# Kernel tuning notes

Measured on AMD Instinct MI355X. Metric: run time of the kernel, lower is better.

## Reference

```python
import jax, jax.numpy as jnp
import numpy as np

NUM_GRAPHS = 4
INPUT_SIZE = 50000          # nodes per graph
BOTTLENECK = 64
FFN = 128
HIDDEN = [1, 8, 16]         # hidden_channels; convs go 16->8 then 8->1
E = 3200000                 # num edges (avg degree 16)
N = NUM_GRAPHS * INPUT_SIZE # total nodes = 200000


def setup_inputs() -> dict:
    key = jax.random.key(0)
    ks = jax.random.split(key, 12)
    d = {}
    d["x"] = jax.random.normal(ks[0], (NUM_GRAPHS, BOTTLENECK), dtype=jnp.float32)
    d["edge_index"] = jax.random.randint(ks[1], (2, E), 0, N, dtype=jnp.int64)
    d["edge_weight"] = jax.random.uniform(ks[2], (E,), dtype=jnp.float32)
    # learned params (stored as [in, out] so forward is x @ W + b)
    d["fc1_w"] = jax.random.normal(ks[3], (BOTTLENECK, FFN), dtype=jnp.float32) / np.sqrt(BOTTLENECK)
    d["fc1_b"] = jnp.zeros((FFN,), dtype=jnp.float32)
    d["fc2_w"] = jax.random.normal(ks[4], (FFN, INPUT_SIZE * HIDDEN[-1]), dtype=jnp.float32) / np.sqrt(FFN)
    d["fc2_b"] = jnp.zeros((INPUT_SIZE * HIDDEN[-1],), dtype=jnp.float32)
    d["conv0_w"] = jax.random.normal(ks[5], (HIDDEN[2], HIDDEN[1]), dtype=jnp.float32) / np.sqrt(HIDDEN[2])
    d["conv0_b"] = jnp.zeros((HIDDEN[1],), dtype=jnp.float32)
    d["conv1_w"] = jax.random.normal(ks[6], (HIDDEN[1], HIDDEN[0]), dtype=jnp.float32) / np.sqrt(HIDDEN[1])
    d["conv1_b"] = jnp.zeros((HIDDEN[0],), dtype=jnp.float32)
    d["num_graphs"] = NUM_GRAPHS
    return d


def _gcn_conv(x, row, col, ew, W, b, n_nodes):
    """PyG GCNConv: add self loops (weight 1), symmetric normalization,
    scatter-add of normalized source features, then linear weight + bias."""
    loop = jnp.arange(n_nodes, dtype=row.dtype)
    r = jnp.concatenate([row, loop])
    c = jnp.concatenate([col, loop])
    w = jnp.concatenate([ew, jnp.ones((n_nodes,), dtype=ew.dtype)])
    deg = jax.ops.segment_sum(w, c, num_segments=n_nodes)          # [N]
    dinv = jnp.where(deg > 0, jax.lax.rsqrt(deg), 0.0)
    norm = dinv[r] * w * dinv[c]                                    # [E+N]
    h = x @ W                                                       # [N, out]
    msg = h[r] * norm[:, None]                                      # gather + scale
    out = jax.ops.segment_sum(msg, c, num_segments=n_nodes)        # scatter-add
    return out + b


def reference(x, edge_index, edge_weight, fc1_w, fc1_b, fc2_w, fc2_b,
              conv0_w, conv0_b, conv1_w, conv1_b, num_graphs):
    act = jax.nn.elu
    row, col = edge_index[0], edge_index[1]
    n_nodes = num_graphs * INPUT_SIZE
    z = act(x @ fc1_w + fc1_b)                                     # [G, ffn]
    z = act(z @ fc2_w + fc2_b)                                     # [G, input_size*hidden[-1]]
    h = z.reshape(n_nodes, HIDDEN[-1])                             # [N, 16]
    out = _gcn_conv(h, row, col, edge_weight, conv0_w, conv0_b, n_nodes)  # 16->8
    out = act(out)                                                 # act except last layer
    out = _gcn_conv(out, row, col, edge_weight, conv1_w, conv1_b, n_nodes)  # 8->1
    return out
```

## Files before the change

kernel.cpp:

```cpp
#include <hip/hip_runtime.h>
#include <cstddef>

#define NGRAPH  4
#define NPG     50000
#define NNODES  200000
#define BNECK   64
#define FFN     128
#define COLS    800000
#define NEDGE   3200000
#define H2      16
#define H1      8

#define MAXDEG  40
#define OVCAP   8192
#define RANGES  16
#define RW      (NNODES / RANGES)
#define EPB     4096
#define CH      ((NEDGE + EPB - 1) / EPB)

#define SCAN_B  512
#define NB      ((NNODES + SCAN_B - 1) / SCAN_B)

__device__ __forceinline__ float elu(float x) {
    return x > 0.f ? x : expm1f(x);
}

__global__ void k_fc1(const float* __restrict__ x, const float* __restrict__ w,
                      const float* __restrict__ b, float* __restrict__ z1) {
    int t = threadIdx.x;
    int g = t >> 7, j = t & 127;
    float acc = b[j];
    #pragma unroll 8
    for (int i = 0; i < BNECK; ++i)
        acc = fmaf(x[g * BNECK + i], w[i * FFN + j], acc);
    z1[t] = elu(acc);
}

__global__ void k_zero(int* __restrict__ p, int n) {
    int i = blockIdx.x * blockDim.x + threadIdx.x;
    if (i < n) p[i] = 0;
}

__global__ void k_place_ell(const int* __restrict__ row, const int* __restrict__ col,
                            const float* __restrict__ ew,
                            int* __restrict__ cnt, int2* __restrict__ ell,
                            int* __restrict__ ovc, int3* __restrict__ ovf) {
    int b = blockIdx.x;
    int x = b & 7;
    int q = b >> 3;
    int p = q / CH;
    int chunk = q - p * CH;
    int c0 = (p * 8 + x) * RW;
    int c1 = c0 + RW;
    int base = chunk * EPB;
    #pragma unroll
    for (int i = 0; i < EPB / 256; ++i) {
        int e = base + i * 256 + threadIdx.x;
        if (e < NEDGE) {
            int c = col[e];
            if (c >= c0 && c < c1) {
                int pos = atomicAdd(&cnt[c], 1);
                if (pos < MAXDEG) {
                    int2 ent; ent.x = row[e]; ent.y = __float_as_int(ew[e]);
                    ell[(size_t)c * MAXDEG + pos] = ent;
                } else {
                    int o = atomicAdd(ovc, 1);
                    if (o < OVCAP) {
                        int3 ent3; ent3.x = c; ent3.y = row[e]; ent3.z = __float_as_int(ew[e]);
                        ovf[o] = ent3;
                    }
                }
            }
        }
    }
}

__global__ void k_deg_ell(const int* __restrict__ cnt, const int2* __restrict__ ell,
                          const int* __restrict__ ovc, const int3* __restrict__ ovf,
                          float* __restrict__ dinv) {
    int n = blockIdx.x * blockDim.x + threadIdx.x;
    if (n >= NNODES) return;
    int d = cnt[n];
    int m = d < MAXDEG ? d : MAXDEG;
    const int2* en = &ell[(size_t)n * MAXDEG];
    float s = 1.0f;
    for (int j = 0; j < m; ++j) s += __int_as_float(en[j].y);
    if (d > MAXDEG) {
        int oc = *ovc; if (oc > OVCAP) oc = OVCAP;
        for (int j = 0; j < oc; ++j)
            if (ovf[j].x == n) s += __int_as_float(ovf[j].z);
    }
    dinv[n] = rsqrtf(s);
}

__global__ __launch_bounds__(256) void k_fc2(
    const float* __restrict__ z1, const float* __restrict__ w2,
    const float* __restrict__ b2, const float* __restrict__ cw0,
    const float* __restrict__ dinv,
    float* __restrict__ hws, float* __restrict__ acc0)
{
    __shared__ float s_z1[NGRAPH * FFN];
    __shared__ float s_cw[H2 * H1];
    __shared__ float s_h[NGRAPH][1024];

    int t = threadIdx.x;
    for (int i = t; i < NGRAPH * FFN; i += 256) s_z1[i] = z1[i];
    if (t < H2 * H1) s_cw[t] = cw0[t];
    __syncthreads();

    int j0 = blockIdx.x * 1024;
    int jj = j0 + t * 4;
    if (jj < COLS) {
        float4 a0 = {0,0,0,0}, a1 = {0,0,0,0}, a2 = {0,0,0,0}, a3 = {0,0,0,0};
        #pragma unroll 4
        for (int i = 0; i < FFN; ++i) {
            const float4 wv = *reinterpret_cast<const float4*>(&w2[(size_t)i * COLS + jj]);
            float zg0 = s_z1[0 * FFN + i];
            float zg1 = s_z1[1 * FFN + i];
            float zg2 = s_z1[2 * FFN + i];
            float zg3 = s_z1[3 * FFN + i];
            a0.x = fmaf(zg0, wv.x, a0.x); a0.y = fmaf(zg0, wv.y, a0.y);
            a0.z = fmaf(zg0, wv.z, a0.z); a0.w = fmaf(zg0, wv.w, a0.w);
            a1.x = fmaf(zg1, wv.x, a1.x); a1.y = fmaf(zg1, wv.y, a1.y);
            a1.z = fmaf(zg1, wv.z, a1.z); a1.w = fmaf(zg1, wv.w, a1.w);
            a2.x = fmaf(zg2, wv.x, a2.x); a2.y = fmaf(zg2, wv.y, a2.y);
            a2.z = fmaf(zg2, wv.z, a2.z); a2.w = fmaf(zg2, wv.w, a2.w);
            a3.x = fmaf(zg3, wv.x, a3.x); a3.y = fmaf(zg3, wv.y, a3.y);
            a3.z = fmaf(zg3, wv.z, a3.z); a3.w = fmaf(zg3, wv.w, a3.w);
        }
        const float4 bv = *reinterpret_cast<const float4*>(&b2[jj]);
        s_h[0][t*4+0] = elu(a0.x + bv.x); s_h[0][t*4+1] = elu(a0.y + bv.y);
        s_h[0][t*4+2] = elu(a0.z + bv.z); s_h[0][t*4+3] = elu(a0.w + bv.w);
        s_h[1][t*4+0] = elu(a1.x + bv.x); s_h[1][t*4+1] = elu(a1.y + bv.y);
        s_h[1][t*4+2] = elu(a1.z + bv.z); s_h[1][t*4+3] = elu(a1.w + bv.w);
        s_h[2][t*4+0] = elu(a2.x + bv.x); s_h[2][t*4+1] = elu(a2.y + bv.y);
        s_h[2][t*4+2] = elu(a2.z + bv.z); s_h[2][t*4+3] = elu(a2.w + bv.w);
        s_h[3][t*4+0] = elu(a3.x + bv.x); s_h[3][t*4+1] = elu(a3.y + bv.y);
        s_h[3][t*4+2] = elu(a3.z + bv.z); s_h[3][t*4+3] = elu(a3.w + bv.w);
    }
    __syncthreads();

    int nbase = j0 >> 4;
    for (int o = t; o < NGRAPH * 64 * H1; o += 256) {
        int g  = o >> 9;
        int lo = o & 511;
        int nl = lo >> 3;
        int m  = lo & 7;
        int nloc = nbase + nl;
        if (nloc < NPG) {
            const float* hr = &s_h[g][nl * 16];
            float s = 0.f;
            #pragma unroll
            for (int k = 0; k < H2; ++k) s = fmaf(hr[k], s_cw[k * H1 + m], s);
            int node = g * NPG + nloc;
            float di = dinv[node];
            hws[node * H1 + m]  = s * di;
            acc0[node * H1 + m] = s * (di * di);
        }
    }
}

__global__ void k_gather0_ell(const int* __restrict__ cnt, const int2* __restrict__ ell,
                              const int* __restrict__ ovc, const int3* __restrict__ ovf,
                              const float* __restrict__ hws, const float* __restrict__ acc0,
                              const float* __restrict__ b0, const float* __restrict__ cw1,
                              const float* __restrict__ dinv, float* __restrict__ h1s) {
    int n = blockIdx.x * blockDim.x + threadIdx.x;
    if (n >= NNODES) return;
    int d = cnt[n];
    int m = d < MAXDEG ? d : MAXDEG;
    const int2* en = &ell[(size_t)n * MAXDEG];
    float4 mA = {0,0,0,0}, mB = {0,0,0,0};
    for (int j = 0; j < m; ++j) {
        int2 ent = en[j];
        float w = __int_as_float(ent.y);
        const float4 ha = *reinterpret_cast<const float4*>(&hws[ent.x * H1]);
        const float4 hb = *reinterpret_cast<const float4*>(&hws[ent.x * H1 + 4]);
        mA.x = fmaf(ha.x, w, mA.x); mA.y = fmaf(ha.y, w, mA.y);
        mA.z = fmaf(ha.z, w, mA.z); mA.w = fmaf(ha.w, w, mA.w);
        mB.x = fmaf(hb.x, w, mB.x); mB.y = fmaf(hb.y, w, mB.y);
        mB.z = fmaf(hb.z, w, mB.z); mB.w = fmaf(hb.w, w, mB.w);
    }
    if (d > MAXDEG) {
        int oc = *ovc; if (oc > OVCAP) oc = OVCAP;
        for (int j = 0; j < oc; ++j) {
            if (ovf[j].x == n) {
                float w = __int_as_float(ovf[j].z);
                int r = ovf[j].y;
                const float4 ha = *reinterpret_cast<const float4*>(&hws[r * H1]);
                const float4 hb = *reinterpret_cast<const float4*>(&hws[r * H1 + 4]);
                mA.x = fmaf(ha.x, w, mA.x); mA.y = fmaf(ha.y, w, mA.y);
                mA.z = fmaf(ha.z, w, mA.z); mA.w = fmaf(ha.w, w, mA.w);
                mB.x = fmaf(hb.x, w, mB.x); mB.y = fmaf(hb.y, w, mB.y);
                mB.z = fmaf(hb.z, w, mB.z); mB.w = fmaf(hb.w, w, mB.w);
            }
        }
    }
    float dc = dinv[n];
    const float4 sA = *reinterpret_cast<const float4*>(&acc0[n * H1]);
    const float4 sB = *reinterpret_cast<const float4*>(&acc0[n * H1 + 4]);
    float s = 0.f;
    s = fmaf(elu(sA.x + dc * mA.x + b0[0]), cw1[0], s);
    s = fmaf(elu(sA.y + dc * mA.y + b0[1]), cw1[1], s);
    s = fmaf(elu(sA.z + dc * mA.z + b0[2]), cw1[2], s);
    s = fmaf(elu(sA.w + dc * mA.w + b0[3]), cw1[3], s);
    s = fmaf(elu(sB.x + dc * mB.x + b0[4]), cw1[4], s);
    s = fmaf(elu(sB.y + dc * mB.y + b0[5]), cw1[5], s);
    s = fmaf(elu(sB.z + dc * mB.z + b0[6]), cw1[6], s);
    s = fmaf(elu(sB.w + dc * mB.w + b0[7]), cw1[7], s);
    h1s[n] = s * dc;
}

__global__ void k_gather1_ell(const int* __restrict__ cnt, const int2* __restrict__ ell,
                              const int* __restrict__ ovc, const int3* __restrict__ ovf,
                              const float* __restrict__ h1s, const float* __restrict__ dinv,
                              const float* __restrict__ cb1, float* __restrict__ out) {
    int n = blockIdx.x * blockDim.x + threadIdx.x;
    if (n >= NNODES) return;
    int d = cnt[n];
    int m = d < MAXDEG ? d : MAXDEG;
    const int2* en = &ell[(size_t)n * MAXDEG];
    float a = h1s[n];
    for (int j = 0; j < m; ++j) {
        int2 ent = en[j];
        a = fmaf(h1s[ent.x], __int_as_float(ent.y), a);
    }
    if (d > MAXDEG) {
        int oc = *ovc; if (oc > OVCAP) oc = OVCAP;
        for (int j = 0; j < oc; ++j)
            if (ovf[j].x == n) a = fmaf(h1s[ovf[j].y], __int_as_float(ovf[j].z), a);
    }
    out[n] = cb1[0] + a * dinv[n];
}

__global__ void k_hist(const int* __restrict__ col, int* __restrict__ cnt) {
    int e = blockIdx.x * blockDim.x + threadIdx.x;
    if (e < NEDGE) atomicAdd(&cnt[col[e]], 1);
}

__global__ void k_bsum(const int* __restrict__ cnt, int* __restrict__ bsum) {
    __shared__ int s[SCAN_B];
    int t = threadIdx.x;
    int i = blockIdx.x * SCAN_B + t;
    s[t] = (i < NNODES) ? cnt[i] : 0;
    __syncthreads();
    for (int st = SCAN_B / 2; st > 0; st >>= 1) {
        if (t < st) s[t] += s[t + st];
        __syncthreads();
    }
    if (t == 0) bsum[blockIdx.x] = s[0];
}

__global__ void k_btop(const int* __restrict__ bsum, int* __restrict__ bstart) {
    __shared__ int s[SCAN_B];
    int t = threadIdx.x;
    int v = (t < NB) ? bsum[t] : 0;
    s[t] = v;
    __syncthreads();
    for (int st = 1; st < SCAN_B; st <<= 1) {
        int x = (t >= st) ? s[t - st] : 0;
        __syncthreads();
        s[t] += x;
        __syncthreads();
    }
    if (t < NB) bstart[t] = s[t] - v;
}

__global__ void k_bscan(int* __restrict__ cnt, const int* __restrict__ bstart) {
    __shared__ int s[SCAN_B];
    int t = threadIdx.x;
    int i = blockIdx.x * SCAN_B + t;
    int v = (i < NNODES) ? cnt[i] : 0;
    s[t] = v;
    __syncthreads();
    for (int st = 1; st < SCAN_B; st <<= 1) {
        int x = (t >= st) ? s[t - st] : 0;
        __syncthreads();
        s[t] += x;
        __syncthreads();
    }
    if (i < NNODES) cnt[i] = bstart[blockIdx.x] + s[t] - v;
}

__global__ void k_place(const int* __restrict__ row, const int* __restrict__ col,
                        const float* __restrict__ ew,
                        int* __restrict__ offs, int2* __restrict__ csr) {
    int e = blockIdx.x * blockDim.x + threadIdx.x;
    if (e >= NEDGE) return;
    int c = col[e];
    int pos = atomicAdd(&offs[c], 1);
    int2 ent;
    ent.x = row[e];
    ent.y = __float_as_int(ew[e]);
    csr[pos] = ent;
}

__global__ void k_deg(const int* __restrict__ offs, const int2* __restrict__ csr,
                      float* __restrict__ dinv) {
    int n = blockIdx.x * blockDim.x + threadIdx.x;
    if (n >= NNODES) return;
    int s0 = n ? offs[n - 1] : 0;
    int e0 = offs[n];
    float d = 1.0f;
    for (int j = s0; j < e0; ++j) d += __int_as_float(csr[j].y);
    dinv[n] = rsqrtf(d);
}

__global__ void k_gather0(const int* __restrict__ offs, const int2* __restrict__ csr,
                          const float* __restrict__ hws, const float* __restrict__ acc0,
                          const float* __restrict__ b0, const float* __restrict__ cw1,
                          const float* __restrict__ dinv, float* __restrict__ h1s) {
    int n = blockIdx.x * blockDim.x + threadIdx.x;
    if (n >= NNODES) return;
    int s0 = n ? offs[n - 1] : 0;
    int e0 = offs[n];
    float4 mA = {0,0,0,0}, mB = {0,0,0,0};
    for (int j = s0; j < e0; ++j) {
        int2 ent = csr[j];
        int   r = ent.x;
        float w = __int_as_float(ent.y);
        const float4 ha = *reinterpret_cast<const float4*>(&hws[r * H1]);
        const float4 hb = *reinterpret_cast<const float4*>(&hws[r * H1 + 4]);
        mA.x = fmaf(ha.x, w, mA.x); mA.y = fmaf(ha.y, w, mA.y);
        mA.z = fmaf(ha.z, w, mA.z); mA.w = fmaf(ha.w, w, mA.w);
        mB.x = fmaf(hb.x, w, mB.x); mB.y = fmaf(hb.y, w, mB.y);
        mB.z = fmaf(hb.z, w, mB.z); mB.w = fmaf(hb.w, w, mB.w);
    }
    float dc = dinv[n];
    const float4 sA = *reinterpret_cast<const float4*>(&acc0[n * H1]);
    const float4 sB = *reinterpret_cast<const float4*>(&acc0[n * H1 + 4]);
    float s = 0.f;
    s = fmaf(elu(sA.x + dc * mA.x + b0[0]), cw1[0], s);
    s = fmaf(elu(sA.y + dc * mA.y + b0[1]), cw1[1], s);
    s = fmaf(elu(sA.z + dc * mA.z + b0[2]), cw1[2], s);
    s = fmaf(elu(sA.w + dc * mA.w + b0[3]), cw1[3], s);
    s = fmaf(elu(sB.x + dc * mB.x + b0[4]), cw1[4], s);
    s = fmaf(elu(sB.y + dc * mB.y + b0[5]), cw1[5], s);
    s = fmaf(elu(sB.z + dc * mB.z + b0[6]), cw1[6], s);
    s = fmaf(elu(sB.w + dc * mB.w + b0[7]), cw1[7], s);
    h1s[n] = s * dc;
}

__global__ void k_gather1(const int* __restrict__ offs, const int2* __restrict__ csr,
                          const float* __restrict__ h1s, const float* __restrict__ dinv,
                          const float* __restrict__ cb1, float* __restrict__ out) {
    int n = blockIdx.x * blockDim.x + threadIdx.x;
    if (n >= NNODES) return;
    int s0 = n ? offs[n - 1] : 0;
    int e0 = offs[n];
    float a = h1s[n];
    for (int j = s0; j < e0; ++j) {
        int2 ent = csr[j];
        a = fmaf(h1s[ent.x], __int_as_float(ent.y), a);
    }
    out[n] = cb1[0] + a * dinv[n];
}

extern "C" void kernel_launch(void* const* d_in, const int* in_sizes, int n_in,
                              void* d_out, int out_size, void* d_ws, size_t ws_size,
                              hipStream_t stream) {
    const float* x    = (const float*)d_in[0];
    const int*   ei   = (const int*)d_in[1];
    const float* ew   = (const float*)d_in[2];
    const float* fc1w = (const float*)d_in[3];
    const float* fc1b = (const float*)d_in[4];
    const float* fc2w = (const float*)d_in[5];
    const float* fc2b = (const float*)d_in[6];
    const float* cw0  = (const float*)d_in[7];
    const float* cb0  = (const float*)d_in[8];
    const float* cw1  = (const float*)d_in[9];
    const float* cb1  = (const float*)d_in[10];
    float* out = (float*)d_out;

    const int* row = ei;
    const int* col = ei + NEDGE;

    float* ws    = (float*)d_ws;
    float* z1    = ws;
    float* dinv  = ws + 512;
    float* hws   = dinv + NNODES;
    float* acc0  = hws + (size_t)NNODES * H1;
    float* h1s   = acc0 + (size_t)NNODES * H1;

    size_t ell_units = 512 + NNODES + 2u * (size_t)NNODES * H1 + NNODES
                     + (NNODES + 8) + (3u * OVCAP) + 2u * (size_t)NNODES * MAXDEG;
    bool use_ell = ws_size >= ell_units * 4u + 256u;

    if (use_ell) {
        int*  cnt = (int*)(h1s + NNODES);
        int*  ovc = cnt + NNODES;
        int3* ovf = (int3*)(ovc + 8);
        int2* ell = (int2*)((int*)ovf + 3 * OVCAP);

        k_fc1 <<<1, 512, 0, stream>>>(x, fc1w, fc1b, z1);
        k_zero<<<(NNODES + 8 + 255) / 256, 256, 0, stream>>>(cnt, NNODES + 8);
        k_place_ell<<<2 * CH * 8, 256, 0, stream>>>(row, col, ew, cnt, ell, ovc, ovf);
        k_deg_ell<<<(NNODES + 255) / 256, 256, 0, stream>>>(cnt, ell, ovc, ovf, dinv);
        k_fc2<<<(COLS + 1023) / 1024, 256, 0, stream>>>(z1, fc2w, fc2b, cw0, dinv, hws, acc0);
        k_gather0_ell<<<(NNODES + 255) / 256, 256, 0, stream>>>(cnt, ell, ovc, ovf, hws, acc0,
                                                                cb0, cw1, dinv, h1s);
        k_gather1_ell<<<(NNODES + 255) / 256, 256, 0, stream>>>(cnt, ell, ovc, ovf, h1s, dinv,
                                                                cb1, out);
    } else {
        int*   offs  = (int*)(h1s + NNODES);
        int*   bsum  = offs + NNODES;
        int*   bst   = bsum + SCAN_B;
        int2*  csr   = (int2*)(bst + SCAN_B);

        k_fc1 <<<1, 512, 0, stream>>>(x, fc1w, fc1b, z1);
        k_zero<<<(NNODES + 255) / 256, 256, 0, stream>>>(offs, NNODES);
        k_hist<<<(NEDGE + 255) / 256, 256, 0, stream>>>(col, offs);
        k_bsum<<<NB, SCAN_B, 0, stream>>>(offs, bsum);
        k_btop<<<1, SCAN_B, 0, stream>>>(bsum, bst);
        k_bscan<<<NB, SCAN_B, 0, stream>>>(offs, bst);
        k_place<<<(NEDGE + 255) / 256, 256, 0, stream>>>(row, col, ew, offs, csr);
        k_deg<<<(NNODES + 255) / 256, 256, 0, stream>>>(offs, csr, dinv);
        k_fc2<<<(COLS + 1023) / 1024, 256, 0, stream>>>(z1, fc2w, fc2b, cw0, dinv, hws, acc0);
        k_gather0<<<(NNODES + 255) / 256, 256, 0, stream>>>(offs, csr, hws, acc0, cb0, cw1, dinv, h1s);
        k_gather1<<<(NNODES + 255) / 256, 256, 0, stream>>>(offs, csr, h1s, dinv, cb1, out);
    }
}
```

Before: 952.1 us.

## Fuse init kernels, accumulate degree atomically, vectorize ELL edge reads

Merges fc1 and the zeroing into one init kernel. Degrees are now accumulated with float atomics during ELL placement, so the separate pass that re-read the ELL table is replaced by a trivial rsqrt kernel. The column reads in placement become int4 loads with larger chunks, and the gather kernels read ELL entries two at a time as int4. MAXDEG shrinks to 32, which saves memory but sends more edges to the overflow list, whose linear scan is costly for high-degree nodes. Float atomic ordering also makes degree sums nondeterministic.

```diff
diff --git a/kernel.cpp b/kernel.cpp
--- a/kernel.cpp
+++ b/kernel.cpp
@@ -11,11 +11,11 @@
 #define H2      16
 #define H1      8
 
-#define MAXDEG  40
+#define MAXDEG  32
 #define OVCAP   8192
 #define RANGES  16
 #define RW      (NNODES / RANGES)
-#define EPB     4096
+#define EPB     8192
 #define CH      ((NEDGE + EPB - 1) / EPB)
 
 #define SCAN_B  512
@@ -25,25 +25,29 @@
     return x > 0.f ? x : expm1f(x);
 }
 
-__global__ void k_fc1(const float* __restrict__ x, const float* __restrict__ w,
-                      const float* __restrict__ b, float* __restrict__ z1) {
-    int t = threadIdx.x;
-    int g = t >> 7, j = t & 127;
-    float acc = b[j];
-    #pragma unroll 8
-    for (int i = 0; i < BNECK; ++i)
-        acc = fmaf(x[g * BNECK + i], w[i * FFN + j], acc);
-    z1[t] = elu(acc);
-}
-
-__global__ void k_zero(int* __restrict__ p, int n) {
-    int i = blockIdx.x * blockDim.x + threadIdx.x;
-    if (i < n) p[i] = 0;
+__global__ void k_init(const float* __restrict__ x, const float* __restrict__ w,
+                       const float* __restrict__ b, float* __restrict__ z1,
+                       int* __restrict__ cnt, float* __restrict__ degf,
+                       int* __restrict__ ovc) {
+    if (blockIdx.x == 0) {
+        int t = threadIdx.x;
+        int g = t >> 7, j = t & 127;
+        float acc = b[j];
+        #pragma unroll 8
+        for (int i = 0; i < BNECK; ++i)
+            acc = fmaf(x[g * BNECK + i], w[i * FFN + j], acc);
+        z1[t] = elu(acc);
+        if (t == 0) *ovc = 0;
+    } else {
+        int i = (blockIdx.x - 1) * 512 + threadIdx.x;
+        if (i < NNODES) { cnt[i] = 0; degf[i] = 1.0f; }
+    }
 }
 
 __global__ void k_place_ell(const int* __restrict__ row, const int* __restrict__ col,
                             const float* __restrict__ ew,
-                            int* __restrict__ cnt, int2* __restrict__ ell,
+                            int* __restrict__ cnt, float* __restrict__ degf,
+                            int2* __restrict__ ell,
                             int* __restrict__ ovc, int3* __restrict__ ovf) {
     int b = blockIdx.x;
     int x = b & 7;
@@ -53,21 +57,29 @@
     int c0 = (p * 8 + x) * RW;
     int c1 = c0 + RW;
     int base = chunk * EPB;
+    const int4* col4 = reinterpret_cast<const int4*>(col);
     #pragma unroll
-    for (int i = 0; i < EPB / 256; ++i) {
-        int e = base + i * 256 + threadIdx.x;
+    for (int i = 0; i < EPB / 1024; ++i) {
+        int e = base + i * 1024 + threadIdx.x * 4;
         if (e < NEDGE) {
-            int c = col[e];
-            if (c >= c0 && c < c1) {
-                int pos = atomicAdd(&cnt[c], 1);
-                if (pos < MAXDEG) {
-                    int2 ent; ent.x = row[e]; ent.y = __float_as_int(ew[e]);
-                    ell[(size_t)c * MAXDEG + pos] = ent;
-                } else {
-                    int o = atomicAdd(ovc, 1);
-                    if (o < OVCAP) {
-                        int3 ent3; ent3.x = c; ent3.y = row[e]; ent3.z = __float_as_int(ew[e]);
-                        ovf[o] = ent3;
+            int4 c4 = col4[e >> 2];
+            #pragma unroll
+            for (int k = 0; k < 4; ++k) {
+                int c = (k == 0) ? c4.x : (k == 1) ? c4.y : (k == 2) ? c4.z : c4.w;
+                if (c >= c0 && c < c1) {
+                    int ee = e + k;
+                    float w = ew[ee];
+                    atomicAdd(&degf[c], w);
+                    int pos = atomicAdd(&cnt[c], 1);
+                    if (pos < MAXDEG) {
+                        int2 ent; ent.x = row[ee]; ent.y = __float_as_int(w);
+                        ell[(size_t)c * MAXDEG + pos] = ent;
+                    } else {
+                        int o = atomicAdd(ovc, 1);
+                        if (o < OVCAP) {
+                            int3 ent3; ent3.x = c; ent3.y = row[ee]; ent3.z = __float_as_int(w);
+                            ovf[o] = ent3;
+                        }
                     }
                 }
             }
@@ -75,22 +87,9 @@
     }
 }
 
-__global__ void k_deg_ell(const int* __restrict__ cnt, const int2* __restrict__ ell,
-                          const int* __restrict__ ovc, const int3* __restrict__ ovf,
-                          float* __restrict__ dinv) {
-    int n = blockIdx.x * blockDim.x + threadIdx.x;
-    if (n >= NNODES) return;
-    int d = cnt[n];
-    int m = d < MAXDEG ? d : MAXDEG;
-    const int2* en = &ell[(size_t)n * MAXDEG];
-    float s = 1.0f;
-    for (int j = 0; j < m; ++j) s += __int_as_float(en[j].y);
-    if (d > MAXDEG) {
-        int oc = *ovc; if (oc > OVCAP) oc = OVCAP;
-        for (int j = 0; j < oc; ++j)
-            if (ovf[j].x == n) s += __int_as_float(ovf[j].z);
-    }
-    dinv[n] = rsqrtf(s);
+__global__ void k_dinv(const float* __restrict__ degf, float* __restrict__ dinv) {
+    int n = blockIdx.x * blockDim.x + threadIdx.x;
+    if (n < NNODES) dinv[n] = rsqrtf(degf[n]);
 }
 
 __global__ __launch_bounds__(256) void k_fc2(
@@ -160,6 +159,16 @@
     }
 }
 
+__device__ __forceinline__ void acc_msg(int r, float w, const float* __restrict__ hws,
+                                        float4& mA, float4& mB) {
+    const float4 ha = *reinterpret_cast<const float4*>(&hws[r * H1]);
+    const float4 hb = *reinterpret_cast<const float4*>(&hws[r * H1 + 4]);
+    mA.x = fmaf(ha.x, w, mA.x); mA.y = fmaf(ha.y, w, mA.y);
+    mA.z = fmaf(ha.z, w, mA.z); mA.w = fmaf(ha.w, w, mA.w);
+    mB.x = fmaf(hb.x, w, mB.x); mB.y = fmaf(hb.y, w, mB.y);
+    mB.z = fmaf(hb.z, w, mB.z); mB.w = fmaf(hb.w, w, mB.w);
+}
+
 __global__ void k_gather0_ell(const int* __restrict__ cnt, const int2* __restrict__ ell,
                               const int* __restrict__ ovc, const int3* __restrict__ ovf,
                               const float* __restrict__ hws, const float* __restrict__ acc0,
@@ -169,32 +178,22 @@
     if (n >= NNODES) return;
     int d = cnt[n];
     int m = d < MAXDEG ? d : MAXDEG;
-    const int2* en = &ell[(size_t)n * MAXDEG];
+    const int4* en4 = reinterpret_cast<const int4*>(&ell[(size_t)n * MAXDEG]);
     float4 mA = {0,0,0,0}, mB = {0,0,0,0};
-    for (int j = 0; j < m; ++j) {
-        int2 ent = en[j];
-        float w = __int_as_float(ent.y);
-        const float4 ha = *reinterpret_cast<const float4*>(&hws[ent.x * H1]);
-        const float4 hb = *reinterpret_cast<const float4*>(&hws[ent.x * H1 + 4]);
-        mA.x = fmaf(ha.x, w, mA.x); mA.y = fmaf(ha.y, w, mA.y);
-        mA.z = fmaf(ha.z, w, mA.z); mA.w = fmaf(ha.w, w, mA.w);
-        mB.x = fmaf(hb.x, w, mB.x); mB.y = fmaf(hb.y, w, mB.y);
-        mB.z = fmaf(hb.z, w, mB.z); mB.w = fmaf(hb.w, w, mB.w);
+    int h = m >> 1;
+    for (int j = 0; j < h; ++j) {
+        int4 pr = en4[j];
+        acc_msg(pr.x, __int_as_float(pr.y), hws, mA, mB);
+        acc_msg(pr.z, __int_as_float(pr.w), hws, mA, mB);
+    }
+    if (m & 1) {
+        int2 ent = ell[(size_t)n * MAXDEG + m - 1];
+        acc_msg(ent.x, __int_as_float(ent.y), hws, mA, mB);
     }
     if (d > MAXDEG) {
         int oc = *ovc; if (oc > OVCAP) oc = OVCAP;
-        for (int j = 0; j < oc; ++j) {
-            if (ovf[j].x == n) {
-                float w = __int_as_float(ovf[j].z);
-                int r = ovf[j].y;
-                const float4 ha = *reinterpret_cast<const float4*>(&hws[r * H1]);
-                const float4 hb = *reinterpret_cast<const float4*>(&hws[r * H1 + 4]);
-                mA.x = fmaf(ha.x, w, mA.x); mA.y = fmaf(ha.y, w, mA.y);
-                mA.z = fmaf(ha.z, w, mA.z); mA.w = fmaf(ha.w, w, mA.w);
-                mB.x = fmaf(hb.x, w, mB.x); mB.y = fmaf(hb.y, w, mB.y);
-                mB.z = fmaf(hb.z, w, mB.z); mB.w = fmaf(hb.w, w, mB.w);
-            }
-        }
+        for (int j = 0; j < oc; ++j)
+            if (ovf[j].x == n) acc_msg(ovf[j].y, __int_as_float(ovf[j].z), hws, mA, mB);
     }
     float dc = dinv[n];
     const float4 sA = *reinterpret_cast<const float4*>(&acc0[n * H1]);
@@ -219,10 +218,16 @@
     if (n >= NNODES) return;
     int d = cnt[n];
     int m = d < MAXDEG ? d : MAXDEG;
-    const int2* en = &ell[(size_t)n * MAXDEG];
+    const int4* en4 = reinterpret_cast<const int4*>(&ell[(size_t)n * MAXDEG]);
     float a = h1s[n];
-    for (int j = 0; j < m; ++j) {
-        int2 ent = en[j];
+    int h = m >> 1;
+    for (int j = 0; j < h; ++j) {
+        int4 pr = en4[j];
+        a = fmaf(h1s[pr.x], __int_as_float(pr.y), a);
+        a = fmaf(h1s[pr.z], __int_as_float(pr.w), a);
+    }
+    if (m & 1) {
+        int2 ent = ell[(size_t)n * MAXDEG + m - 1];
         a = fmaf(h1s[ent.x], __int_as_float(ent.y), a);
     }
     if (d > MAXDEG) {
@@ -231,6 +236,22 @@
             if (ovf[j].x == n) a = fmaf(h1s[ovf[j].y], __int_as_float(ovf[j].z), a);
     }
     out[n] = cb1[0] + a * dinv[n];
+}
+
+__global__ void k_fc1(const float* __restrict__ x, const float* __restrict__ w,
+                      const float* __restrict__ b, float* __restrict__ z1) {
+    int t = threadIdx.x;
+    int g = t >> 7, j = t & 127;
+    float acc = b[j];
+    #pragma unroll 8
+    for (int i = 0; i < BNECK; ++i)
+        acc = fmaf(x[g * BNECK + i], w[i * FFN + j], acc);
+    z1[t] = elu(acc);
+}
+
+__global__ void k_zero(int* __restrict__ p, int n) {
+    int i = blockIdx.x * blockDim.x + threadIdx.x;
+    if (i < n) p[i] = 0;
 }
 
 __global__ void k_hist(const int* __restrict__ col, int* __restrict__ cnt) {
@@ -317,14 +338,7 @@
     float4 mA = {0,0,0,0}, mB = {0,0,0,0};
     for (int j = s0; j < e0; ++j) {
         int2 ent = csr[j];
-        int   r = ent.x;
-        float w = __int_as_float(ent.y);
-        const float4 ha = *reinterpret_cast<const float4*>(&hws[r * H1]);
-        const float4 hb = *reinterpret_cast<const float4*>(&hws[r * H1 + 4]);
-        mA.x = fmaf(ha.x, w, mA.x); mA.y = fmaf(ha.y, w, mA.y);
-        mA.z = fmaf(ha.z, w, mA.z); mA.w = fmaf(ha.w, w, mA.w);
-        mB.x = fmaf(hb.x, w, mB.x); mB.y = fmaf(hb.y, w, mB.y);
-        mB.z = fmaf(hb.z, w, mB.z); mB.w = fmaf(hb.w, w, mB.w);
+        acc_msg(ent.x, __int_as_float(ent.y), hws, mA, mB);
     }
     float dc = dinv[n];
     const float4 sA = *reinterpret_cast<const float4*>(&acc0[n * H1]);
@@ -383,19 +397,20 @@
     float* h1s   = acc0 + (size_t)NNODES * H1;
 
     size_t ell_units = 512 + NNODES + 2u * (size_t)NNODES * H1 + NNODES
-                     + (NNODES + 8) + (3u * OVCAP) + 2u * (size_t)NNODES * MAXDEG;
+                     + NNODES + NNODES + 8 + (3u * OVCAP)
+                     + 2u * (size_t)NNODES * MAXDEG;
     bool use_ell = ws_size >= ell_units * 4u + 256u;
 
     if (use_ell) {
-        int*  cnt = (int*)(h1s + NNODES);
-        int*  ovc = cnt + NNODES;
-        int3* ovf = (int3*)(ovc + 8);
-        int2* ell = (int2*)((int*)ovf + 3 * OVCAP);
-
-        k_fc1 <<<1, 512, 0, stream>>>(x, fc1w, fc1b, z1);
-        k_zero<<<(NNODES + 8 + 255) / 256, 256, 0, stream>>>(cnt, NNODES + 8);
-        k_place_ell<<<2 * CH * 8, 256, 0, stream>>>(row, col, ew, cnt, ell, ovc, ovf);
-        k_deg_ell<<<(NNODES + 255) / 256, 256, 0, stream>>>(cnt, ell, ovc, ovf, dinv);
+        int*   cnt  = (int*)(h1s + NNODES);
+        float* degf = (float*)(cnt + NNODES);
+        int*   ovc  = (int*)(degf + NNODES);
+        int3*  ovf  = (int3*)(ovc + 8);
+        int2*  ell  = (int2*)((int*)ovf + 3 * OVCAP);
+
+        k_init<<<1 + (NNODES + 511) / 512, 512, 0, stream>>>(x, fc1w, fc1b, z1, cnt, degf, ovc);
+        k_place_ell<<<2 * CH * 8, 256, 0, stream>>>(row, col, ew, cnt, degf, ell, ovc, ovf);
+        k_dinv<<<(NNODES + 255) / 256, 256, 0, stream>>>(degf, dinv);
         k_fc2<<<(COLS + 1023) / 1024, 256, 0, stream>>>(z1, fc2w, fc2b, cw0, dinv, hws, acc0);
         k_gather0_ell<<<(NNODES + 255) / 256, 256, 0, stream>>>(cnt, ell, ovc, ovf, hws, acc0,
                                                                 cb0, cw1, dinv, h1s);
```

Result: slower. 1.021 ms (+7.2%).
